# Kernel optimization log

Hardware: AMD Instinct MI355X
Metric: run time of the kernel (lower is better)

Reference implementation:

```python
import jax, jax.numpy as jnp
import numpy as np
import math

B, S, H = 4, 2048, 1024


def setup_inputs() -> dict:
    key = jax.random.key(0)
    ks = jax.random.split(key, 9)
    scale = 1.0 / math.sqrt(H)
    x = jax.random.normal(ks[0], (B, S, H), dtype=jnp.float32)
    attention_mask = jax.random.randint(ks[1], (B, S, S), 0, 2, dtype=jnp.int32)
    Wq = jax.random.uniform(ks[2], (H, H), jnp.float32, -scale, scale)
    bq = jax.random.uniform(ks[3], (H,), jnp.float32, -scale, scale)
    Wk = jax.random.uniform(ks[4], (H, H), jnp.float32, -scale, scale)
    bk = jax.random.uniform(ks[5], (H,), jnp.float32, -scale, scale)
    Wv = jax.random.uniform(ks[6], (H, H), jnp.float32, -scale, scale)
    bv = jax.random.uniform(ks[7], (H,), jnp.float32, -scale, scale)
    return {"x": x, "attention_mask": attention_mask,
            "Wq": Wq, "bq": bq, "Wk": Wk, "bk": bk, "Wv": Wv, "bv": bv}


def reference(x, attention_mask, Wq, bq, Wk, bk, Wv, bv):
    # q/k/v projections (torch Linear: x @ W.T + b)
    q = jnp.einsum('bsh,oh->bso', x, Wq) + bq
    k = jnp.einsum('bsh,oh->bso', x, Wk) + bk
    v = jnp.einsum('bsh,oh->bso', x, Wv) + bv
    # raw scores [B,S,S]
    scores = jnp.einsum('bqh,bkh->bqk', q, k)
    # NOTE: faithful to original - mask fill happens BEFORE the 1/sqrt(H) scaling
    scores = jnp.where(attention_mask == 0, jnp.float32(-1e9), scores)
    attn = jax.nn.softmax(scores / math.sqrt(H), axis=-1)
    # dropout p=0.0 (eval mode) -> identity
    return jnp.einsum('bqk,bkh->bqh', attn, v)
```

## Files before the change

kernel.cpp:

```cpp
#include <hip/hip_runtime.h>

#define B_ 4
#define S_ 2048
#define H_ 1024

typedef __bf16 bf16x8 __attribute__((ext_vector_type(8)));
typedef float  f32x4  __attribute__((ext_vector_type(4)));
typedef short  short8 __attribute__((ext_vector_type(8)));

__device__ __forceinline__ unsigned short f2bf(float f) {
  unsigned u = __float_as_uint(f);
  u += 0x7FFF + ((u >> 16) & 1);
  return (unsigned short)(u >> 16);
}

__global__ void cvt_all_kernel(const float* __restrict__ x,
                               const float* __restrict__ wq,
                               const float* __restrict__ wk,
                               const float* __restrict__ wv,
                               unsigned short* __restrict__ dst) {
  int i = blockIdx.x * blockDim.x + threadIdx.x;
  const int NX = (B_ * S_ * H_) / 4;
  const int NW = (H_ * H_) / 4;
  const float* src; int off;
  if (i < NX) { src = x; off = i; }
  else { int j = i - NX; int w = j >> 18; off = j & (NW - 1);
         src = (w == 0) ? wq : (w == 1) ? wk : wv; }
  float4 v = reinterpret_cast<const float4*>(src)[off];
  ushort4 o; o.x = f2bf(v.x); o.y = f2bf(v.y); o.z = f2bf(v.z); o.w = f2bf(v.w);
  reinterpret_cast<ushort4*>(dst)[i] = o;
}

__global__ void maskpack_kernel(const int* __restrict__ mask,
                                unsigned long long* __restrict__ mpk) {
  const int lane = threadIdx.x & 63;
  const long row = (long)blockIdx.x * 4 + (threadIdx.x >> 6);
  const int* mrow = mask + row * S_;
#pragma unroll
  for (int w = 0; w < S_ / 64; ++w) {
    int v = mrow[w * 64 + lane];
    unsigned long long b = __ballot(v != 0);
    if (lane == 0) mpk[row * (S_ / 64) + w] = b;
  }
}

__device__ __forceinline__ bf16x8 lfrag(const char* base, int row, int kb) {
  return *reinterpret_cast<const bf16x8*>(base + row * 128 + (kb ^ ((row & 7) << 4)));
}

__device__ __forceinline__ void stage_q(const unsigned short* __restrict__ g,
                                        long row0, long ld, int k0e,
                                        char* sbase, int q, int t) {
  int row = q * 64 + (t >> 3);
  int osw = ((t & 7) << 4) ^ ((row & 7) << 4);
  const char* gp = reinterpret_cast<const char*>(g + (row0 + row) * ld + k0e) + osw;
  char* lp = sbase + q * 8192 + ((t >> 6) << 10);
  __builtin_amdgcn_global_load_lds((const __attribute__((address_space(1))) void*)gp,
                                   (__attribute__((address_space(3))) void*)lp,
                                   16, 0, 0);
}

template <int NT>
__device__ __forceinline__ void gemm8(const unsigned short* __restrict__ A, long ldA, long m0,
                                      const unsigned short* __restrict__ Bm, long ldB, long n0,
                                      char* sm, f32x4 acc[8][4]) {
  const int t = threadIdx.x;
  const int lane = t & 63;
  const int wid = t >> 6;
  const int wr = wid >> 2, wc = wid & 3;
  const int lrow = lane & 15;
  const int kb0 = (lane >> 4) * 16;
  char* sA0 = sm;          char* sB0 = sm + 32768;
  char* sA1 = sm + 65536;  char* sB1 = sm + 98304;

#pragma unroll
  for (int q = 0; q < 4; ++q) stage_q(A, m0, ldA, 0, sA0, q, t);
#pragma unroll
  for (int q = 0; q < 4; ++q) stage_q(Bm, n0, ldB, 0, sB0, q, t);
#pragma unroll
  for (int q = 0; q < 4; ++q) stage_q(Bm, n0, ldB, 64, sB1, q, t);
  stage_q(A, m0, ldA, 64, sA1, 0, t);
  stage_q(A, m0, ldA, 64, sA1, 2, t);
  asm volatile("s_waitcnt vmcnt(6)" ::: "memory");
  __builtin_amdgcn_s_barrier();

  auto ktile = [&](int kt, char* cA, char* cB, char* nA) {
    const int k1 = (kt + 1 < NT ? kt + 1 : NT - 1) * 64;
    const int k2 = (kt + 2 < NT ? kt + 2 : NT - 1) * 64;
    bf16x8 bfr[4][2], af[2][2];
#pragma unroll
    for (int nf = 0; nf < 4; ++nf)
#pragma unroll
      for (int ks = 0; ks < 2; ++ks)
        bfr[nf][ks] = lfrag(cB, wc * 64 + nf * 16 + lrow, ks * 64 + kb0);
#pragma unroll
    for (int mf = 0; mf < 2; ++mf)
#pragma unroll
      for (int ks = 0; ks < 2; ++ks)
        af[mf][ks] = lfrag(cA, wr * 128 + mf * 16 + lrow, ks * 64 + kb0);
    stage_q(A, m0, ldA, k1, nA, 1, t);
    stage_q(A, m0, ldA, k1, nA, 3, t);
    __builtin_amdgcn_s_barrier();
    asm volatile("s_waitcnt lgkmcnt(0)" ::: "memory");
    __builtin_amdgcn_sched_barrier(0);
    __builtin_amdgcn_s_setprio(1);
#pragma unroll
    for (int mf = 0; mf < 2; ++mf)
#pragma unroll
      for (int nf = 0; nf < 4; ++nf)
#pragma unroll
        for (int ks = 0; ks < 2; ++ks)
          acc[mf][nf] = __builtin_amdgcn_mfma_f32_16x16x32_bf16(af[mf][ks], bfr[nf][ks], acc[mf][nf], 0, 0, 0);
    __builtin_amdgcn_s_setprio(0);
    __builtin_amdgcn_s_barrier();
#pragma unroll
    for (int q = 1; q < 4; ++q) {
#pragma unroll
      for (int mf = 0; mf < 2; ++mf)
#pragma unroll
        for (int ks = 0; ks < 2; ++ks)
          af[mf][ks] = lfrag(cA, wr * 128 + q * 32 + mf * 16 + lrow, ks * 64 + kb0);
      if (q == 1) { stage_q(Bm, n0, ldB, k2, cB, 0, t); stage_q(Bm, n0, ldB, k2, cB, 1, t); }
      if (q == 2) { stage_q(Bm, n0, ldB, k2, cB, 2, t); stage_q(Bm, n0, ldB, k2, cB, 3, t); }
      if (q == 3) { stage_q(A, m0, ldA, k2, cA, 0, t); stage_q(A, m0, ldA, k2, cA, 2, t);
                    asm volatile("s_waitcnt vmcnt(6)" ::: "memory"); }
      __builtin_amdgcn_s_barrier();
      asm volatile("s_waitcnt lgkmcnt(0)" ::: "memory");
      __builtin_amdgcn_sched_barrier(0);
      __builtin_amdgcn_s_setprio(1);
#pragma unroll
      for (int mf = 0; mf < 2; ++mf)
#pragma unroll
        for (int nf = 0; nf < 4; ++nf)
#pragma unroll
          for (int ks = 0; ks < 2; ++ks)
            acc[2 * q + mf][nf] = __builtin_amdgcn_mfma_f32_16x16x32_bf16(af[mf][ks], bfr[nf][ks], acc[2 * q + mf][nf], 0, 0, 0);
      __builtin_amdgcn_s_setprio(0);
      __builtin_amdgcn_s_barrier();
    }
  };

#pragma unroll 1
  for (int kt = 0; kt < NT; kt += 2) {
    ktile(kt,     sA0, sB0, sA1);
    ktile(kt + 1, sA1, sB1, sA0);
  }
}

#define EPI_PITCH 68

__global__ __launch_bounds__(512, 2) void qkv_kernel(
    const unsigned short* __restrict__ x, const unsigned short* __restrict__ W3,
    const float* __restrict__ bq, const float* __restrict__ bk, const float* __restrict__ bv,
    unsigned short* __restrict__ Q, unsigned short* __restrict__ K, unsigned short* __restrict__ VT) {
  extern __shared__ char sm[];
  const int z = blockIdx.z;
  const unsigned short* W = W3 + (size_t)z * (H_ * H_);
  const float* bias = (z == 0) ? bq : (z == 1) ? bk : bv;
  const long m0 = (long)blockIdx.y * 256, n0 = (long)blockIdx.x * 256;
  f32x4 acc[8][4] = {};
  gemm8<H_ / 64>(x, H_, m0, W, H_, n0, sm, acc);

  const int lane = threadIdx.x & 63;
  const int wid = threadIdx.x >> 6;
  const int wr = wid >> 2, wc = wid & 3;
  const int g = lane >> 4, c = lane & 15;
  float bb[4];
#pragma unroll
  for (int nf = 0; nf < 4; ++nf) bb[nf] = bias[n0 + wc * 64 + nf * 16 + c];

  if (z == 2) {
#pragma unroll
    for (int mq = 0; mq < 8; ++mq)
#pragma unroll
      for (int nf = 0; nf < 4; ++nf) {
        long col = n0 + wc * 64 + nf * 16 + c;
        long row0 = m0 + wr * 128 + mq * 16 + g * 4;
        long bidx = row0 >> 11;
        long srow = row0 & (S_ - 1);
        ushort4 o;
        o.x = f2bf(acc[mq][nf][0] + bb[nf]);
        o.y = f2bf(acc[mq][nf][1] + bb[nf]);
        o.z = f2bf(acc[mq][nf][2] + bb[nf]);
        o.w = f2bf(acc[mq][nf][3] + bb[nf]);
        *reinterpret_cast<ushort4*>(VT + bidx * H_ * S_ + col * S_ + srow) = o;
      }
  } else {
    unsigned short* out = (z == 0) ? Q : K;
    float* wbuf = reinterpret_cast<float*>(sm) + wid * (32 * EPI_PITCH);
#pragma unroll
    for (int p = 0; p < 4; ++p) {
#pragma unroll
      for (int h2 = 0; h2 < 2; ++h2)
#pragma unroll
        for (int nf = 0; nf < 4; ++nf)
#pragma unroll
          for (int r = 0; r < 4; ++r)
            wbuf[(h2 * 16 + g * 4 + r) * EPI_PITCH + nf * 16 + c] = acc[p * 2 + h2][nf][r] + bb[nf];
      asm volatile("s_waitcnt lgkmcnt(0)" ::: "memory");
      __builtin_amdgcn_sched_barrier(0);
#pragma unroll
      for (int it = 0; it < 4; ++it) {
        int lr = it * 8 + (lane >> 3);
        long row = m0 + wr * 128 + p * 32 + lr;
        const float* src = wbuf + lr * EPI_PITCH + (lane & 7) * 8;
        float4 v0 = *reinterpret_cast<const float4*>(src);
        float4 v1 = *reinterpret_cast<const float4*>(src + 4);
        short8 o;
        o[0] = f2bf(v0.x); o[1] = f2bf(v0.y); o[2] = f2bf(v0.z); o[3] = f2bf(v0.w);
        o[4] = f2bf(v1.x); o[5] = f2bf(v1.y); o[6] = f2bf(v1.z); o[7] = f2bf(v1.w);
        *reinterpret_cast<short8*>(out + row * H_ + n0 + wc * 64 + (lane & 7) * 8) = o;
      }
    }
  }
}

__global__ __launch_bounds__(512, 2) void scores_kernel(
    const unsigned short* __restrict__ Q, const unsigned short* __restrict__ Km,
    const unsigned char* __restrict__ mpkb, unsigned short* __restrict__ P,
    float* __restrict__ rowsum) {
  extern __shared__ char sm[];
  const int b = blockIdx.z;
  const long m0 = (long)blockIdx.y * 256, n0 = (long)blockIdx.x * 256;
  const unsigned short* Qb = Q + (size_t)b * S_ * H_;
  const unsigned short* Kb = Km + (size_t)b * S_ * H_;
  const unsigned char* Mb = mpkb + (size_t)b * S_ * (S_ / 8);
  unsigned short* Pb = P + (size_t)b * S_ * S_;
  f32x4 acc[8][4] = {};
  gemm8<H_ / 64>(Qb, H_, m0, Kb, H_, n0, sm, acc);

  const int lane = threadIdx.x & 63;
  const int wid = threadIdx.x >> 6;
  const int wr = wid >> 2, wc = wid & 3;
  const int g = lane >> 4, c = lane & 15;
  float* wbuf = reinterpret_cast<float*>(sm) + wid * (32 * EPI_PITCH);
#pragma unroll
  for (int p = 0; p < 4; ++p) {
#pragma unroll
    for (int h2 = 0; h2 < 2; ++h2)
#pragma unroll
      for (int nf = 0; nf < 4; ++nf)
#pragma unroll
        for (int r = 0; r < 4; ++r)
          wbuf[(h2 * 16 + g * 4 + r) * EPI_PITCH + nf * 16 + c] = acc[p * 2 + h2][nf][r];
    asm volatile("s_waitcnt lgkmcnt(0)" ::: "memory");
    __builtin_amdgcn_sched_barrier(0);
#pragma unroll
    for (int it = 0; it < 4; ++it) {
      int lr = it * 8 + (lane >> 3);
      long row = m0 + wr * 128 + p * 32 + lr;
      const float* src = wbuf + lr * EPI_PITCH + (lane & 7) * 8;
      float4 v0 = *reinterpret_cast<const float4*>(src);
      float4 v1 = *reinterpret_cast<const float4*>(src + 4);
      unsigned mb = Mb[row * (S_ / 8) + ((n0 + wc * 64) >> 3) + (lane & 7)];
      float pv[8];
      pv[0] = v0.x; pv[1] = v0.y; pv[2] = v0.z; pv[3] = v0.w;
      pv[4] = v1.x; pv[5] = v1.y; pv[6] = v1.z; pv[7] = v1.w;
      float rs = 0.f;
      short8 o;
#pragma unroll
      for (int j = 0; j < 8; ++j) {
        float pj = ((mb >> j) & 1) ? __expf(pv[j] * 0.03125f) : 0.f;
        rs += pj;
        o[j] = (short)f2bf(pj);
      }
      *reinterpret_cast<short8*>(Pb + row * S_ + n0 + wc * 64 + (lane & 7) * 8) = o;
      rs += __shfl_xor(rs, 1, 64);
      rs += __shfl_xor(rs, 2, 64);
      rs += __shfl_xor(rs, 4, 64);
      if ((lane & 7) == 0) atomicAdd(&rowsum[(size_t)b * S_ + row], rs);
    }
  }
}

__global__ __launch_bounds__(512, 2) void pv_kernel(
    const unsigned short* __restrict__ P, const unsigned short* __restrict__ VT,
    const float* __restrict__ rowsum, float* __restrict__ out) {
  extern __shared__ char sm[];
  const int b = blockIdx.z;
  const long m0 = (long)blockIdx.y * 256, n0 = (long)blockIdx.x * 256;
  const unsigned short* Pb = P + (size_t)b * S_ * S_;
  const unsigned short* VTb = VT + (size_t)b * H_ * S_;
  f32x4 acc[8][4] = {};
  gemm8<S_ / 64>(Pb, S_, m0, VTb, S_, n0, sm, acc);

  const int lane = threadIdx.x & 63;
  const int wid = threadIdx.x >> 6;
  const int wr = wid >> 2, wc = wid & 3;
  const int g = lane >> 4, c = lane & 15;
  float* wbuf = reinterpret_cast<float*>(sm) + wid * (32 * EPI_PITCH);
#pragma unroll
  for (int p = 0; p < 4; ++p) {
#pragma unroll
    for (int h2 = 0; h2 < 2; ++h2)
#pragma unroll
      for (int nf = 0; nf < 4; ++nf)
#pragma unroll
        for (int r = 0; r < 4; ++r)
          wbuf[(h2 * 16 + g * 4 + r) * EPI_PITCH + nf * 16 + c] = acc[p * 2 + h2][nf][r];
    asm volatile("s_waitcnt lgkmcnt(0)" ::: "memory");
    __builtin_amdgcn_sched_barrier(0);
#pragma unroll
    for (int it = 0; it < 8; ++it) {
      int lr = it * 4 + (lane >> 4);
      long row = m0 + wr * 128 + p * 32 + lr;
      float inv = __frcp_rn(rowsum[(size_t)b * S_ + row]);
      const float* src = wbuf + lr * EPI_PITCH + (lane & 15) * 4;
      float4 v = *reinterpret_cast<const float4*>(src);
      float4 o; o.x = v.x * inv; o.y = v.y * inv; o.z = v.z * inv; o.w = v.w * inv;
      *reinterpret_cast<float4*>(out + ((size_t)b * S_ + row) * H_ + n0 + wc * 64 + (lane & 15) * 4) = o;
    }
  }
}

extern "C" void kernel_launch(void* const* d_in, const int* in_sizes, int n_in,
                              void* d_out, int out_size, void* d_ws, size_t ws_size,
                              hipStream_t stream) {
  const float* x   = (const float*)d_in[0];
  const int* mask  = (const int*)d_in[1];
  const float* Wq  = (const float*)d_in[2];
  const float* bq  = (const float*)d_in[3];
  const float* Wk  = (const float*)d_in[4];
  const float* bk  = (const float*)d_in[5];
  const float* Wv  = (const float*)d_in[6];
  const float* bv  = (const float*)d_in[7];
  float* out = (float*)d_out;

  const size_t MS = (size_t)B_ * S_ * H_;
  unsigned short* xb  = (unsigned short*)d_ws;
  unsigned short* W3  = xb + MS;
  unsigned short* Qb  = W3 + (size_t)3 * H_ * H_;
  unsigned short* Kb  = Qb + MS;
  unsigned short* VTb = Kb + MS;
  unsigned short* Pb  = VTb + MS;
  float* rowsum = (float*)(Pb + (size_t)B_ * S_ * S_);
  unsigned long long* mpk = (unsigned long long*)(rowsum + B_ * S_);

  (void)hipFuncSetAttribute(reinterpret_cast<const void*>(qkv_kernel),
                            hipFuncAttributeMaxDynamicSharedMemorySize, 131072);
  (void)hipFuncSetAttribute(reinterpret_cast<const void*>(scores_kernel),
                            hipFuncAttributeMaxDynamicSharedMemorySize, 131072);
  (void)hipFuncSetAttribute(reinterpret_cast<const void*>(pv_kernel),
                            hipFuncAttributeMaxDynamicSharedMemorySize, 131072);

  hipMemsetAsync(rowsum, 0, (size_t)B_ * S_ * sizeof(float), stream);

  const int NCVT = (int)(MS / 4) + 3 * (H_ * H_ / 4);
  cvt_all_kernel<<<NCVT / 256, 256, 0, stream>>>(x, Wq, Wk, Wv, xb);

  maskpack_kernel<<<(B_ * S_) / 4, 256, 0, stream>>>(mask, mpk);

  qkv_kernel<<<dim3(H_ / 256, (B_ * S_) / 256, 3), 512, 131072, stream>>>(
      xb, W3, bq, bk, bv, Qb, Kb, VTb);

  scores_kernel<<<dim3(S_ / 256, S_ / 256, B_), 512, 131072, stream>>>(
      Qb, Kb, (const unsigned char*)mpk, Pb, rowsum);

  pv_kernel<<<dim3(H_ / 256, S_ / 256, B_), 512, 131072, stream>>>(Pb, VTb, rowsum, out);
}
```

Measured before the change: 320.1 us.

## Narrow PV tile to 256x128, add XCD-aware block remap, drain loads before epilogue

The GEMM core is templated on the number of B-fragment columns, so the PV kernel can use 256x128 output tiles. This doubles its grid (256 blocks for 256 CUs) and improves occupancy and load balance, with a matching retuned load schedule and epilogue layout. All three GEMM kernels also remap block indices so that neighbouring tiles land on the same XCD, aiming for better L2 reuse. A full vmcnt drain plus barrier is added after the main loop so the epilogue cannot overwrite LDS that in-flight prefetches still target, at the cost of one extra sync.

```diff
diff --git a/kernel.cpp b/kernel.cpp
--- a/kernel.cpp
+++ b/kernel.cpp
@@ -12,6 +12,13 @@
   unsigned u = __float_as_uint(f);
   u += 0x7FFF + ((u >> 16) & 1);
   return (unsigned short)(u >> 16);
+}
+
+__device__ __forceinline__ void xcd_remap(int& bx, int& by, int gx, int nwg) {
+  int lin = by * gx + bx;
+  int q = nwg >> 3;
+  int nl = (lin & 7) * q + (lin >> 3);
+  bx = nl % gx; by = nl / gx;
 }
 
 __global__ void cvt_all_kernel(const float* __restrict__ x,
@@ -60,10 +67,10 @@
                                    16, 0, 0);
 }
 
-template <int NT>
+template <int NT, int NB>
 __device__ __forceinline__ void gemm8(const unsigned short* __restrict__ A, long ldA, long m0,
                                       const unsigned short* __restrict__ Bm, long ldB, long n0,
-                                      char* sm, f32x4 acc[8][4]) {
+                                      char* sm, f32x4 (&acc)[8][NB]) {
   const int t = threadIdx.x;
   const int lane = t & 63;
   const int wid = t >> 6;
@@ -76,23 +83,24 @@
 #pragma unroll
   for (int q = 0; q < 4; ++q) stage_q(A, m0, ldA, 0, sA0, q, t);
 #pragma unroll
-  for (int q = 0; q < 4; ++q) stage_q(Bm, n0, ldB, 0, sB0, q, t);
-#pragma unroll
-  for (int q = 0; q < 4; ++q) stage_q(Bm, n0, ldB, 64, sB1, q, t);
+  for (int q = 0; q < NB; ++q) stage_q(Bm, n0, ldB, 0, sB0, q, t);
+#pragma unroll
+  for (int q = 0; q < NB; ++q) stage_q(Bm, n0, ldB, 64, sB1, q, t);
   stage_q(A, m0, ldA, 64, sA1, 0, t);
   stage_q(A, m0, ldA, 64, sA1, 2, t);
-  asm volatile("s_waitcnt vmcnt(6)" ::: "memory");
+  if constexpr (NB == 4) asm volatile("s_waitcnt vmcnt(6)" ::: "memory");
+  else                   asm volatile("s_waitcnt vmcnt(4)" ::: "memory");
   __builtin_amdgcn_s_barrier();
 
   auto ktile = [&](int kt, char* cA, char* cB, char* nA) {
     const int k1 = (kt + 1 < NT ? kt + 1 : NT - 1) * 64;
     const int k2 = (kt + 2 < NT ? kt + 2 : NT - 1) * 64;
-    bf16x8 bfr[4][2], af[2][2];
-#pragma unroll
-    for (int nf = 0; nf < 4; ++nf)
+    bf16x8 bfr[NB][2], af[2][2];
+#pragma unroll
+    for (int nf = 0; nf < NB; ++nf)
 #pragma unroll
       for (int ks = 0; ks < 2; ++ks)
-        bfr[nf][ks] = lfrag(cB, wc * 64 + nf * 16 + lrow, ks * 64 + kb0);
+        bfr[nf][ks] = lfrag(cB, wc * (NB * 16) + nf * 16 + lrow, ks * 64 + kb0);
 #pragma unroll
     for (int mf = 0; mf < 2; ++mf)
 #pragma unroll
@@ -107,7 +115,7 @@
 #pragma unroll
     for (int mf = 0; mf < 2; ++mf)
 #pragma unroll
-      for (int nf = 0; nf < 4; ++nf)
+      for (int nf = 0; nf < NB; ++nf)
 #pragma unroll
         for (int ks = 0; ks < 2; ++ks)
           acc[mf][nf] = __builtin_amdgcn_mfma_f32_16x16x32_bf16(af[mf][ks], bfr[nf][ks], acc[mf][nf], 0, 0, 0);
@@ -121,9 +129,14 @@
         for (int ks = 0; ks < 2; ++ks)
           af[mf][ks] = lfrag(cA, wr * 128 + q * 32 + mf * 16 + lrow, ks * 64 + kb0);
       if (q == 1) { stage_q(Bm, n0, ldB, k2, cB, 0, t); stage_q(Bm, n0, ldB, k2, cB, 1, t); }
-      if (q == 2) { stage_q(Bm, n0, ldB, k2, cB, 2, t); stage_q(Bm, n0, ldB, k2, cB, 3, t); }
-      if (q == 3) { stage_q(A, m0, ldA, k2, cA, 0, t); stage_q(A, m0, ldA, k2, cA, 2, t);
-                    asm volatile("s_waitcnt vmcnt(6)" ::: "memory"); }
+      if constexpr (NB == 4) {
+        if (q == 2) { stage_q(Bm, n0, ldB, k2, cB, 2, t); stage_q(Bm, n0, ldB, k2, cB, 3, t); }
+        if (q == 3) { stage_q(A, m0, ldA, k2, cA, 0, t); stage_q(A, m0, ldA, k2, cA, 2, t);
+                      asm volatile("s_waitcnt vmcnt(6)" ::: "memory"); }
+      } else {
+        if (q == 2) { stage_q(A, m0, ldA, k2, cA, 0, t); stage_q(A, m0, ldA, k2, cA, 2, t); }
+        if (q == 3) { asm volatile("s_waitcnt vmcnt(4)" ::: "memory"); }
+      }
       __builtin_amdgcn_s_barrier();
       asm volatile("s_waitcnt lgkmcnt(0)" ::: "memory");
       __builtin_amdgcn_sched_barrier(0);
@@ -131,7 +144,7 @@
 #pragma unroll
       for (int mf = 0; mf < 2; ++mf)
 #pragma unroll
-        for (int nf = 0; nf < 4; ++nf)
+        for (int nf = 0; nf < NB; ++nf)
 #pragma unroll
           for (int ks = 0; ks < 2; ++ks)
             acc[2 * q + mf][nf] = __builtin_amdgcn_mfma_f32_16x16x32_bf16(af[mf][ks], bfr[nf][ks], acc[2 * q + mf][nf], 0, 0, 0);
@@ -145,6 +158,8 @@
     ktile(kt,     sA0, sB0, sA1);
     ktile(kt + 1, sA1, sB1, sA0);
   }
+  asm volatile("s_waitcnt vmcnt(0)" ::: "memory");
+  __syncthreads();
 }
 
 #define EPI_PITCH 68
@@ -154,12 +169,14 @@
     const float* __restrict__ bq, const float* __restrict__ bk, const float* __restrict__ bv,
     unsigned short* __restrict__ Q, unsigned short* __restrict__ K, unsigned short* __restrict__ VT) {
   extern __shared__ char sm[];
+  int bx = blockIdx.x, by = blockIdx.y;
+  xcd_remap(bx, by, H_ / 256, (H_ / 256) * ((B_ * S_) / 256));
   const int z = blockIdx.z;
   const unsigned short* W = W3 + (size_t)z * (H_ * H_);
   const float* bias = (z == 0) ? bq : (z == 1) ? bk : bv;
-  const long m0 = (long)blockIdx.y * 256, n0 = (long)blockIdx.x * 256;
+  const long m0 = (long)by * 256, n0 = (long)bx * 256;
   f32x4 acc[8][4] = {};
-  gemm8<H_ / 64>(x, H_, m0, W, H_, n0, sm, acc);
+  gemm8<H_ / 64, 4>(x, H_, m0, W, H_, n0, sm, acc);
 
   const int lane = threadIdx.x & 63;
   const int wid = threadIdx.x >> 6;
@@ -220,14 +237,16 @@
     const unsigned char* __restrict__ mpkb, unsigned short* __restrict__ P,
     float* __restrict__ rowsum) {
   extern __shared__ char sm[];
+  int bx = blockIdx.x, by = blockIdx.y;
+  xcd_remap(bx, by, S_ / 256, (S_ / 256) * (S_ / 256));
   const int b = blockIdx.z;
-  const long m0 = (long)blockIdx.y * 256, n0 = (long)blockIdx.x * 256;
+  const long m0 = (long)by * 256, n0 = (long)bx * 256;
   const unsigned short* Qb = Q + (size_t)b * S_ * H_;
   const unsigned short* Kb = Km + (size_t)b * S_ * H_;
   const unsigned char* Mb = mpkb + (size_t)b * S_ * (S_ / 8);
   unsigned short* Pb = P + (size_t)b * S_ * S_;
   f32x4 acc[8][4] = {};
-  gemm8<H_ / 64>(Qb, H_, m0, Kb, H_, n0, sm, acc);
+  gemm8<H_ / 64, 4>(Qb, H_, m0, Kb, H_, n0, sm, acc);
 
   const int lane = threadIdx.x & 63;
   const int wid = threadIdx.x >> 6;
@@ -277,38 +296,40 @@
     const unsigned short* __restrict__ P, const unsigned short* __restrict__ VT,
     const float* __restrict__ rowsum, float* __restrict__ out) {
   extern __shared__ char sm[];
+  int bx = blockIdx.x, by = blockIdx.y;
+  xcd_remap(bx, by, H_ / 128, (H_ / 128) * (S_ / 256));
   const int b = blockIdx.z;
-  const long m0 = (long)blockIdx.y * 256, n0 = (long)blockIdx.x * 256;
+  const long m0 = (long)by * 256, n0 = (long)bx * 128;
   const unsigned short* Pb = P + (size_t)b * S_ * S_;
   const unsigned short* VTb = VT + (size_t)b * H_ * S_;
-  f32x4 acc[8][4] = {};
-  gemm8<S_ / 64>(Pb, S_, m0, VTb, S_, n0, sm, acc);
+  f32x4 acc[8][2] = {};
+  gemm8<S_ / 64, 2>(Pb, S_, m0, VTb, S_, n0, sm, acc);
 
   const int lane = threadIdx.x & 63;
   const int wid = threadIdx.x >> 6;
   const int wr = wid >> 2, wc = wid & 3;
   const int g = lane >> 4, c = lane & 15;
-  float* wbuf = reinterpret_cast<float*>(sm) + wid * (32 * EPI_PITCH);
+  float* wbuf = reinterpret_cast<float*>(sm) + wid * (32 * 36);
 #pragma unroll
   for (int p = 0; p < 4; ++p) {
 #pragma unroll
     for (int h2 = 0; h2 < 2; ++h2)
 #pragma unroll
-      for (int nf = 0; nf < 4; ++nf)
+      for (int nf = 0; nf < 2; ++nf)
 #pragma unroll
         for (int r = 0; r < 4; ++r)
-          wbuf[(h2 * 16 + g * 4 + r) * EPI_PITCH + nf * 16 + c] = acc[p * 2 + h2][nf][r];
+          wbuf[(h2 * 16 + g * 4 + r) * 36 + nf * 16 + c] = acc[p * 2 + h2][nf][r];
     asm volatile("s_waitcnt lgkmcnt(0)" ::: "memory");
     __builtin_amdgcn_sched_barrier(0);
 #pragma unroll
-    for (int it = 0; it < 8; ++it) {
-      int lr = it * 4 + (lane >> 4);
+    for (int it = 0; it < 4; ++it) {
+      int lr = it * 8 + (lane >> 3);
       long row = m0 + wr * 128 + p * 32 + lr;
       float inv = __frcp_rn(rowsum[(size_t)b * S_ + row]);
-      const float* src = wbuf + lr * EPI_PITCH + (lane & 15) * 4;
+      const float* src = wbuf + lr * 36 + (lane & 7) * 4;
       float4 v = *reinterpret_cast<const float4*>(src);
       float4 o; o.x = v.x * inv; o.y = v.y * inv; o.z = v.z * inv; o.w = v.w * inv;
-      *reinterpret_cast<float4*>(out + ((size_t)b * S_ + row) * H_ + n0 + wc * 64 + (lane & 15) * 4) = o;
+      *reinterpret_cast<float4*>(out + ((size_t)b * S_ + row) * H_ + n0 + wc * 32 + (lane & 7) * 4) = o;
     }
   }
 }
@@ -356,5 +377,5 @@
   scores_kernel<<<dim3(S_ / 256, S_ / 256, B_), 512, 131072, stream>>>(
       Qb, Kb, (const unsigned char*)mpk, Pb, rowsum);
 
-  pv_kernel<<<dim3(H_ / 256, S_ / 256, B_), 512, 131072, stream>>>(Pb, VTb, rowsum, out);
-}
+  pv_kernel<<<dim3(H_ / 128, S_ / 256, B_), 512, 131072, stream>>>(Pb, VTb, rowsum, out);
+}
```

After: 300.2 us. 1.07x faster.
